# Performance work log

Measured on AMD Instinct MI355X. Metric: run time of the kernel, lower is better.

## Reference

```python
import jax, jax.numpy as jnp
import numpy as np

B, SEQ_LEN, ENC_IN, C_OUT = 128, 512, 21, 21
PRED_LEN, D_MODEL, N_HEADS, D_FF = 96, 512, 8, 2048
E_LAYERS = 2
PATCH_LEN, STRIDE = 16, 8
NUM_PATCH = (SEQ_LEN - PATCH_LEN) // STRIDE + 1  # 63
MODES = min(32, NUM_PATCH // 2)  # 31 (mode_select='low' -> index = range(MODES))
K_MA = 25
EPS = 1e-5
DH = D_MODEL // N_HEADS  # 64


def setup_inputs() -> dict:
    key = jax.random.key(0)
    ks = jax.random.split(key, 16)
    s = 0.02
    fscale = 1.0 / (D_MODEL * D_MODEL)
    return {
        'x_enc': jax.random.normal(ks[0], (B, SEQ_LEN, ENC_IN), jnp.float32),
        'x_mark_enc': jax.random.normal(ks[1], (B, SEQ_LEN, 4), jnp.float32),
        'x_dec': jax.random.normal(ks[2], (B, 144, ENC_IN), jnp.float32),
        'x_mark_dec': jax.random.normal(ks[3], (B, 144, 4), jnp.float32),
        'patch_W': s * jax.random.normal(ks[4], (D_MODEL, PATCH_LEN * ENC_IN), jnp.float32),
        'patch_b': jnp.zeros((D_MODEL,), jnp.float32),
        'Wq': s * jax.random.normal(ks[5], (E_LAYERS, D_MODEL, D_MODEL), jnp.float32),
        'bq': jnp.zeros((E_LAYERS, D_MODEL), jnp.float32),
        'Wo': s * jax.random.normal(ks[6], (E_LAYERS, D_MODEL, D_MODEL), jnp.float32),
        'bo': jnp.zeros((E_LAYERS, D_MODEL), jnp.float32),
        'four_wr': fscale * jax.random.uniform(ks[7], (E_LAYERS, N_HEADS, DH, DH, MODES), jnp.float32),
        'four_wi': fscale * jax.random.uniform(ks[8], (E_LAYERS, N_HEADS, DH, DH, MODES), jnp.float32),
        'conv1_W': s * jax.random.normal(ks[9], (E_LAYERS, D_FF, D_MODEL), jnp.float32),
        'conv2_W': s * jax.random.normal(ks[10], (E_LAYERS, D_MODEL, D_FF), jnp.float32),
        'norm_gamma': jnp.ones((D_MODEL,), jnp.float32),
        'norm_beta': jnp.zeros((D_MODEL,), jnp.float32),
        'head_W': s * jax.random.normal(ks[11], (PRED_LEN * C_OUT, NUM_PATCH * D_MODEL), jnp.float32),
        'head_b': jnp.zeros((PRED_LEN * C_OUT,), jnp.float32),
        'trend_W': s * jax.random.normal(ks[12], (PRED_LEN, SEQ_LEN), jnp.float32),
        'trend_b': jnp.zeros((PRED_LEN,), jnp.float32),
    }


def series_decomp(x, k=K_MA):
    # x: [B, L, C]; replicate-pad ends by (k-1)//2, moving mean via cumsum
    pad = (k - 1) // 2
    front = jnp.repeat(x[:, :1, :], pad, axis=1)
    end = jnp.repeat(x[:, -1:, :], pad, axis=1)
    xp = jnp.concatenate([front, x, end], axis=1)
    c = jnp.cumsum(xp, axis=1)
    c = jnp.concatenate([jnp.zeros_like(c[:, :1]), c], axis=1)
    mean = (c[:, k:] - c[:, :-k]) / k
    return x - mean, mean


def my_layernorm(x, g, b):
    mu = x.mean(-1, keepdims=True)
    var = ((x - mu) ** 2).mean(-1, keepdims=True)
    xh = (x - mu) / jnp.sqrt(var + EPS) * g + b
    return xh - xh.mean(axis=1, keepdims=True)


def fourier_block(q, wr, wi):
    # q: [B, L, H, E] -> torch FourierBlock (low-freq modes 0..MODES-1)
    Bq, L, H, E = q.shape
    xs = q.transpose(0, 2, 3, 1)                       # [B,H,E,L]
    x_ft = jnp.fft.rfft(xs, axis=-1)                   # [B,H,E,L//2+1]
    W = wr + 1j * wi                                   # [H,E,F,M] complex
    out_sel = jnp.einsum('bhem,hefm->bhfm', x_ft[..., :MODES], W)
    out_ft = jnp.zeros(x_ft.shape, x_ft.dtype).at[..., :MODES].set(out_sel)
    y = jnp.fft.irfft(out_ft, n=L, axis=-1)            # [B,H,E,L]
    # torch does out.view(B, L, -1) on contiguous [B,H,E,L]; flat reshape is identical
    return y.reshape(Bq, L, H * E)


def encoder_layer(x, Wq_l, bq_l, Wo_l, bo_l, wr, wi, c1, c2):
    Bq, L, D = x.shape
    q = (x @ Wq_l.T + bq_l).reshape(Bq, L, N_HEADS, DH)
    new_x = fourier_block(q, wr, wi) @ Wo_l.T + bo_l
    x, _ = series_decomp(x + new_x)
    y = jax.nn.gelu(x @ c1.T, approximate=False) @ c2.T  # conv1d k=1 == matmul, no bias
    res, _ = series_decomp(x + y)
    return res


def _forward(x_enc, patch_W, patch_b, Wq, bq, Wo, bo, four_wr, four_wi,
             conv1_W, conv2_W, norm_gamma, norm_beta, head_W, head_b, trend_W, trend_b):
    seasonal, trend = series_decomp(x_enc)
    # trend_projection over time axis: [B,L,C] -> [B,P,C]
    trend_out = jnp.einsum('blc,pl->bpc', trend, trend_W) + trend_b[None, :, None]
    # patching (unfold over time per channel, then mix channels)
    xs = seasonal.transpose(0, 2, 1)                   # [B,N,L]
    idx = STRIDE * jnp.arange(NUM_PATCH)[:, None] + jnp.arange(PATCH_LEN)[None, :]
    xp = xs[:, :, idx]                                 # [B,N,P,plen]
    xp = xp.transpose(0, 2, 1, 3).reshape(B, NUM_PATCH, ENC_IN * PATCH_LEN)
    enc = xp @ patch_W.T + patch_b                     # [B,P,D]
    for l in range(E_LAYERS):
        enc = encoder_layer(enc, Wq[l], bq[l], Wo[l], bo[l],
                            four_wr[l], four_wi[l], conv1_W[l], conv2_W[l])
    enc = my_layernorm(enc, norm_gamma, norm_beta)
    seasonal_out = (enc.reshape(B, -1) @ head_W.T + head_b).reshape(B, PRED_LEN, C_OUT)
    return seasonal_out + trend_out


def reference(x_enc, x_mark_enc, x_dec, x_mark_dec, patch_W, patch_b, Wq, bq, Wo, bo,
              four_wr, four_wi, conv1_W, conv2_W, norm_gamma, norm_beta,
              head_W, head_b, trend_W, trend_b):
    # x_mark_enc / x_dec / x_mark_dec are accepted but unused, as in the torch forward
    return _forward(x_enc, patch_W, patch_b, Wq, bq, Wo, bo, four_wr, four_wi,
                    conv1_W, conv2_W, norm_gamma, norm_beta, head_W, head_b, trend_W, trend_b)
```

## Files before the change

### kernel.cpp

```cpp
#include <hip/hip_runtime.h>
#include <math.h>

#define B_ 128
#define T_ 512
#define C_ 21
#define L_ 63
#define D_ 512
#define H_ 8
#define DH_ 64
#define MODES_ 31
#define FF_ 2048
#define P_ 96
#define KMA 25
#define PAD 12
#define NOUT (P_*C_)
#define KHEAD (L_*D_)
#define ML (B_*L_)

typedef __attribute__((ext_vector_type(8))) short short8;
typedef __attribute__((ext_vector_type(4))) float f32x4;

__device__ __forceinline__ unsigned short f2b(float f) {
    union { float f; unsigned u; } v; v.f = f;
    unsigned r = v.u + 0x7FFFu + ((v.u >> 16) & 1u);
    return (unsigned short)(r >> 16);
}
__device__ __forceinline__ float b2f(unsigned short u) {
    union { unsigned u; float f; } v; v.u = ((unsigned)u) << 16;
    return v.f;
}
__device__ __forceinline__ void gld_lds16(const void* g, void* l) {
    __builtin_amdgcn_global_load_lds(
        (const __attribute__((address_space(1))) unsigned int*)g,
        (__attribute__((address_space(3))) unsigned int*)l, 16, 0, 0);
}

__global__ void prep_k(const float* __restrict__ Wq, const float* __restrict__ Wo,
                       const float* __restrict__ c1, const float* __restrict__ c2,
                       unsigned short* __restrict__ WqB, unsigned short* __restrict__ WoB,
                       unsigned short* __restrict__ c1B, unsigned short* __restrict__ c2B,
                       const float* __restrict__ pW, unsigned short* __restrict__ pWB,
                       float* __restrict__ cosT, float* __restrict__ sinT) {
    int i = blockIdx.x * 256 + threadIdx.x;
    if (i < 262144) {
        const float* src = (i < 131072) ? Wq : Wo;
        unsigned short* dst = (i < 131072) ? WqB : WoB;
        int j = i & 131071;
        float4 v = ((const float4*)src)[j];
        uint2 p; p.x = (unsigned)f2b(v.x) | ((unsigned)f2b(v.y) << 16);
        p.y = (unsigned)f2b(v.z) | ((unsigned)f2b(v.w) << 16);
        ((uint2*)dst)[j] = p;
    } else if (i < 1310720) {
        int j = i - 262144;
        const float* src = (j < 524288) ? c1 : c2;
        unsigned short* dst = (j < 524288) ? c1B : c2B;
        j &= 524287;
        float4 v = ((const float4*)src)[j];
        uint2 p; p.x = (unsigned)f2b(v.x) | ((unsigned)f2b(v.y) << 16);
        p.y = (unsigned)f2b(v.z) | ((unsigned)f2b(v.w) << 16);
        ((uint2*)dst)[j] = p;
    } else if (i < 1359872) {
        int j = i - 1310720;
        int row = j / 96, c4 = j % 96;
        uint2 p; p.x = 0; p.y = 0;
        if (c4 < 84) {
            float4 v = *(const float4*)(pW + (size_t)row * 336 + c4 * 4);
            p.x = (unsigned)f2b(v.x) | ((unsigned)f2b(v.y) << 16);
            p.y = (unsigned)f2b(v.z) | ((unsigned)f2b(v.w) << 16);
        }
        ((uint2*)pWB)[j] = p;
    } else if (i < 1361888) {
        int j = i - 1359872;
        int m = j / 63, l = j % 63;
        if (m >= MODES_) { cosT[j] = 0.f; sinT[j] = 0.f; }
        else {
            int r = (m * l) % 63;
            double a = 6.283185307179586476925286766559 * (double)r / 63.0;
            cosT[j] = (float)cos(a); sinT[j] = (float)sin(a);
        }
    }
}

__global__ void decomp_input_k(const float* __restrict__ x,
                               unsigned short* __restrict__ seasB,
                               unsigned short* __restrict__ trendB) {
    int idx = blockIdx.x * 256 + threadIdx.x;
    if (idx >= B_ * C_ * 16) return;
    int tc = idx & 15; int rc = idx >> 4; int c = rc % C_; int b = rc / C_;
    const float* xb = x + (size_t)b * T_ * C_ + c;
    int t0 = tc * 32;
    float sum = 0.f;
    #pragma unroll
    for (int i = -PAD; i <= PAD; ++i) {
        int tt = t0 + i; tt = tt < 0 ? 0 : (tt > T_-1 ? T_-1 : tt);
        sum += xb[(size_t)tt * C_];
    }
    for (int t = t0; t < t0 + 32; ++t) {
        float mean = sum * (1.f / KMA);
        float xv = xb[(size_t)t * C_];
        size_t o = ((size_t)b * T_ + t) * C_ + c;
        seasB[o]  = f2b(xv - mean);
        trendB[o] = f2b(mean);
        int add = t + 13 > T_-1 ? T_-1 : t + 13;
        int rem = t - 12 < 0 ? 0 : t - 12;
        sum += xb[(size_t)add * C_] - xb[(size_t)rem * C_];
    }
}

__global__ void patches_k(const unsigned short* __restrict__ seasB,
                          unsigned short* __restrict__ xpB) {
    int idx = blockIdx.x * 256 + threadIdx.x;
    if (idx >= B_*L_*384) return;
    int col = idx % 384; int r = idx / 384; int n = r % L_; int b = r / L_;
    unsigned short v = 0;
    if (col < 336) {
        int c = col >> 4; int j = col & 15;
        v = seasB[((size_t)b * T_ + 8*n + j) * C_ + c];
    }
    xpB[idx] = v;
}

__global__ __launch_bounds__(256) void trend_mfma(
    const unsigned short* __restrict__ trendB, const float* __restrict__ tW,
    const float* __restrict__ tb, const float* __restrict__ hb,
    float* __restrict__ outT)
{
    __shared__ unsigned short Asl[64*32];
    __shared__ unsigned short Wsl[96*32];
    int bm = blockIdx.x;
    int t = threadIdx.x, wave = t >> 6, lane = t & 63;
    int wr = wave >> 1, wc = wave & 1, g2 = lane >> 4, rl = lane & 15;
    f32x4 acc[2][3] = {};
    int ar = t >> 2, aslot = t & 3;
    int rowg = bm*64 + ar; int ab = rowg / 21, ac = rowg % 21;
    for (int k0 = 0; k0 < 512; k0 += 32) {
        __syncthreads();
        {
            unsigned short vals[8];
            int kb = k0 + aslot*8;
            #pragma unroll
            for (int j = 0; j < 8; ++j)
                vals[j] = trendB[((size_t)ab * T_ + kb + j) * C_ + ac];
            int phys = aslot ^ ((ar>>1)&3);
            *(uint4*)&Asl[ar*32 + phys*8] = *(const uint4*)vals;
        }
        #pragma unroll
        for (int i = 0; i < 3; ++i) {
            int idx = t + 256*i;
            int r = idx >> 3, c4 = idx & 7;
            float4 w4 = *(const float4*)(tW + (size_t)r * T_ + k0 + c4*4);
            uint2 p; p.x = (unsigned)f2b(w4.x) | ((unsigned)f2b(w4.y) << 16);
            p.y = (unsigned)f2b(w4.z) | ((unsigned)f2b(w4.w) << 16);
            *(uint2*)&Wsl[r*32 + (((c4>>1) ^ ((r>>1)&3)) << 3) + ((c4&1) << 2)] = p;
        }
        __syncthreads();
        short8 af[2], wf[3];
        #pragma unroll
        for (int m = 0; m < 2; ++m) {
            int r = wr*32 + m*16 + rl;
            af[m] = *(const short8*)&Asl[r*32 + ((g2 ^ ((r>>1)&3)) << 3)];
        }
        #pragma unroll
        for (int n = 0; n < 3; ++n) {
            int r = wc*48 + n*16 + rl;
            wf[n] = *(const short8*)&Wsl[r*32 + ((g2 ^ ((r>>1)&3)) << 3)];
        }
        #pragma unroll
        for (int m = 0; m < 2; ++m)
            #pragma unroll
            for (int n = 0; n < 3; ++n)
                acc[m][n] = __builtin_amdgcn_mfma_f32_16x16x32_bf16(af[m], wf[n], acc[m][n], 0,0,0);
    }
    #pragma unroll
    for (int n = 0; n < 3; ++n) {
        int p = wc*48 + n*16 + rl;
        float bias = tb[p];
        #pragma unroll
        for (int m = 0; m < 2; ++m)
            #pragma unroll
            for (int j = 0; j < 4; ++j) {
                int rg = bm*64 + wr*32 + m*16 + g2*4 + j;
                int b = rg / 21, c = rg % 21;
                outT[(size_t)b * NOUT + p*21 + c] = acc[m][n][j] + bias + hb[p*21 + c];
            }
    }
}

__global__ __launch_bounds__(256) void gemm_mfma(
    const unsigned short* __restrict__ A,
    const unsigned short* __restrict__ W,
    const float* __restrict__ bias,
    float* __restrict__ Cf,
    unsigned short* __restrict__ Cb,
    int M, int N, int K, int act)
{
    __shared__ unsigned short Asl[64*64];
    __shared__ unsigned short Wsl[128*64];
    int bm = blockIdx.y, bn = blockIdx.x;
    int t = threadIdx.x;
    int wave = t >> 6, lane = t & 63;
    int wr = wave >> 1, wc = wave & 1;
    int g2 = lane >> 4, rl = lane & 15;
    int lr8 = lane >> 3, l7 = lane & 7;
    f32x4 acc[2][4] = {};
    const unsigned short* Ab = A + (size_t)(bm*64) * K;
    const unsigned short* Wb = W + (size_t)(bn*128) * K;

    for (int k0 = 0; k0 < K; k0 += 64) {
        __syncthreads();
        #pragma unroll
        for (int i = 0; i < 2; ++i) {
            int seg = wave*2 + i;
            int r = seg*8 + lr8;
            int ko = (l7 ^ (r & 7)) << 3;
            gld_lds16(Ab + (size_t)r*K + k0 + ko, &Asl[seg*512]);
        }
        #pragma unroll
        for (int i = 0; i < 4; ++i) {
            int seg = wave*4 + i;
            int r = seg*8 + lr8;
            int ko = (l7 ^ (r & 7)) << 3;
            gld_lds16(Wb + (size_t)r*K + k0 + ko, &Wsl[seg*512]);
        }
        __syncthreads();
        short8 af[2][2], wf[2][4];
        #pragma unroll
        for (int sub = 0; sub < 2; ++sub) {
            #pragma unroll
            for (int m = 0; m < 2; ++m) {
                int r = wr*32 + m*16 + rl;
                af[sub][m] = *(const short8*)&Asl[r*64 + (((sub*4+g2) ^ (r&7)) << 3)];
            }
            #pragma unroll
            for (int n = 0; n < 4; ++n) {
                int r = wc*64 + n*16 + rl;
                wf[sub][n] = *(const short8*)&Wsl[r*64 + (((sub*4+g2) ^ (r&7)) << 3)];
            }
        }
        #pragma unroll
        for (int sub = 0; sub < 2; ++sub)
            #pragma unroll
            for (int m = 0; m < 2; ++m)
                #pragma unroll
                for (int n = 0; n < 4; ++n)
                    acc[m][n] = __builtin_amdgcn_mfma_f32_16x16x32_bf16(af[sub][m], wf[sub][n], acc[m][n], 0,0,0);
    }

    int crow0 = bm*64 + wr*32;
    int ccol0 = bn*128 + wc*64;
    #pragma unroll
    for (int n = 0; n < 4; ++n) {
        int col = ccol0 + n*16 + rl;
        float bv = bias ? bias[col] : 0.f;
        #pragma unroll
        for (int m = 0; m < 2; ++m) {
            #pragma unroll
            for (int j = 0; j < 4; ++j) {
                int row = crow0 + m*16 + g2*4 + j;
                float x = acc[m][n][j] + bv;
                if (act == 1) x = 0.5f * x * (1.f + erff(x * 0.70710678118654752f));
                size_t ix = (size_t)row * N + col;
                if (Cf) Cf[ix] = x;
                if (Cb) Cb[ix] = f2b(x);
            }
        }
    }
}

__global__ __launch_bounds__(256) void fourier1_k(
    const float* __restrict__ q, const float* __restrict__ cosT, const float* __restrict__ sinT,
    float* __restrict__ Xre_g, float* __restrict__ Xim_g)
{
    __shared__ float qs[63][64];
    __shared__ float ct[2016], st[2016];
    int b = blockIdx.x >> 3, h = blockIdx.x & 7;
    int t = threadIdx.x;
    for (int idx = t; idx < 1008; idx += 256) {
        int l = idx >> 4, e4 = idx & 15;
        *(float4*)&qs[l][e4*4] = *(const float4*)(q + ((size_t)(b*63 + l))*512 + h*64 + e4*4);
    }
    for (int idx = t; idx < 504; idx += 256) {
        *(float4*)&ct[idx*4] = *(const float4*)(cosT + idx*4);
        *(float4*)&st[idx*4] = *(const float4*)(sinT + idx*4);
    }
    __syncthreads();
    int mm = t & 31, g = t >> 5;
    float re[8] = {}, im[8] = {};
    for (int l = 0; l < 63; ++l) {
        float c = ct[mm*63 + l], s = st[mm*63 + l];
        #pragma unroll
        for (int j = 0; j < 8; ++j) {
            float v = qs[l][g*8 + j];
            re[j] = fmaf(v, c, re[j]);
            im[j] = fmaf(-v, s, im[j]);
        }
    }
    if (mm < MODES_) {
        size_t base = ((size_t)(h*MODES_ + mm)*128 + b)*64 + g*8;
        *(float4*)&Xre_g[base]   = *(float4*)&re[0];
        *(float4*)&Xre_g[base+4] = *(float4*)&re[4];
        *(float4*)&Xim_g[base]   = *(float4*)&im[0];
        *(float4*)&Xim_g[base+4] = *(float4*)&im[4];
    }
}

__global__ __launch_bounds__(256) void fourier2_k(
    const float* __restrict__ Xre_g, const float* __restrict__ Xim_g,
    const float* __restrict__ wr, const float* __restrict__ wi,
    float* __restrict__ Ore_g, float* __restrict__ Oim_g)
{
    __shared__ unsigned short Xr[128*64], Xi[128*64];
    __shared__ unsigned short Wr[64*64], Wi[64*64], Wn[64*64];
    int h = blockIdx.x / MODES_, mm = blockIdx.x % MODES_;
    int t = threadIdx.x;
    size_t xbase = ((size_t)(h*MODES_ + mm)) * 128 * 64;
    #pragma unroll
    for (int i = 0; i < 8; ++i) {
        int idx = t + 256*i;
        int r = idx >> 4, c4 = idx & 15;
        int ad = r*64 + (((c4>>1) ^ (r&7)) << 3) + ((c4&1) << 2);
        float4 v = *(const float4*)(Xre_g + xbase + (size_t)r*64 + c4*4);
        uint2 p; p.x = (unsigned)f2b(v.x) | ((unsigned)f2b(v.y) << 16);
        p.y = (unsigned)f2b(v.z) | ((unsigned)f2b(v.w) << 16);
        *(uint2*)&Xr[ad] = p;
        v = *(const float4*)(Xim_g + xbase + (size_t)r*64 + c4*4);
        p.x = (unsigned)f2b(v.x) | ((unsigned)f2b(v.y) << 16);
        p.y = (unsigned)f2b(v.z) | ((unsigned)f2b(v.w) << 16);
        *(uint2*)&Xi[ad] = p;
    }
    #pragma unroll
    for (int i = 0; i < 2; ++i) {
        int idx = t + 256*i;
        int f = idx >> 3, oct = idx & 7;
        unsigned short wrv[8], wiv[8], wnv[8];
        #pragma unroll
        for (int j = 0; j < 8; ++j) {
            int e = oct*8 + j;
            size_t a = (((size_t)(h*64 + e))*64 + f)*MODES_ + mm;
            wrv[j] = f2b(wr[a]);
            wiv[j] = f2b(wi[a]);
            wnv[j] = wiv[j] ^ 0x8000u;
        }
        int ad = f*64 + ((oct ^ (f&7)) << 3);
        *(uint4*)&Wr[ad] = *(const uint4*)wrv;
        *(uint4*)&Wi[ad] = *(const uint4*)wiv;
        *(uint4*)&Wn[ad] = *(const uint4*)wnv;
    }
    __syncthreads();
    int wave = t >> 6, lane = t & 63;
    int wv = wave >> 1, wc = wave & 1;
    int g2 = lane >> 4, rl = lane & 15;
    f32x4 ar[4][2] = {}, ai[4][2] = {};
    #pragma unroll
    for (int sub = 0; sub < 2; ++sub) {
        short8 xr[4], xi[4], br[2], bi[2], bn[2];
        #pragma unroll
        for (int m = 0; m < 4; ++m) {
            int r = wv*64 + m*16 + rl;
            int off = r*64 + (((sub*4+g2) ^ (r&7)) << 3);
            xr[m] = *(const short8*)&Xr[off];
            xi[m] = *(const short8*)&Xi[off];
        }
        #pragma unroll
        for (int n = 0; n < 2; ++n) {
            int r = wc*32 + n*16 + rl;
            int off = r*64 + (((sub*4+g2) ^ (r&7)) << 3);
            br[n] = *(const short8*)&Wr[off];
            bi[n] = *(const short8*)&Wi[off];
            bn[n] = *(const short8*)&Wn[off];
        }
        #pragma unroll
        for (int m = 0; m < 4; ++m)
            #pragma unroll
            for (int n = 0; n < 2; ++n) {
                ar[m][n] = __builtin_amdgcn_mfma_f32_16x16x32_bf16(xr[m], br[n], ar[m][n], 0,0,0);
                ar[m][n] = __builtin_amdgcn_mfma_f32_16x16x32_bf16(xi[m], bn[n], ar[m][n], 0,0,0);
                ai[m][n] = __builtin_amdgcn_mfma_f32_16x16x32_bf16(xr[m], bi[n], ai[m][n], 0,0,0);
                ai[m][n] = __builtin_amdgcn_mfma_f32_16x16x32_bf16(xi[m], br[n], ai[m][n], 0,0,0);
            }
    }
    #pragma unroll
    for (int m = 0; m < 4; ++m)
        #pragma unroll
        for (int n = 0; n < 2; ++n)
            #pragma unroll
            for (int j = 0; j < 4; ++j) {
                int b = wv*64 + m*16 + g2*4 + j;
                int f = wc*32 + n*16 + rl;
                Ore_g[xbase + (size_t)b*64 + f] = ar[m][n][j];
                Oim_g[xbase + (size_t)b*64 + f] = ai[m][n][j];
            }
}

__global__ __launch_bounds__(256) void fourier3_k(
    const float* __restrict__ Ore_g, const float* __restrict__ Oim_g,
    const float* __restrict__ cosT, const float* __restrict__ sinT,
    unsigned short* __restrict__ yB)
{
    __shared__ float Ore[31][64], Oim[31][64];
    __shared__ float ct[2016], st[2016];
    int b = blockIdx.x >> 3, h = blockIdx.x & 7;
    int t = threadIdx.x;
    for (int idx = t; idx < 496; idx += 256) {
        int m = idx >> 4, e4 = idx & 15;
        size_t a = ((size_t)(h*MODES_ + m)*128 + b)*64 + e4*4;
        *(float4*)&Ore[m][e4*4] = *(const float4*)(Ore_g + a);
        *(float4*)&Oim[m][e4*4] = *(const float4*)(Oim_g + a);
    }
    for (int idx = t; idx < 504; idx += 256) {
        *(float4*)&ct[idx*4] = *(const float4*)(cosT + idx*4);
        *(float4*)&st[idx*4] = *(const float4*)(sinT + idx*4);
    }
    __syncthreads();
    int f = t & 63, w = t >> 6;
    int l0 = w*16;
    float y[16];
    float r0 = Ore[0][f];
    #pragma unroll
    for (int i = 0; i < 16; ++i) y[i] = r0;
    for (int m = 1; m < MODES_; ++m) {
        float re2 = 2.f*Ore[m][f], im2 = 2.f*Oim[m][f];
        #pragma unroll
        for (int i = 0; i < 16; ++i) {
            y[i] = fmaf(re2, ct[m*63 + l0 + i], y[i]);
            y[i] = fmaf(-im2, st[m*63 + l0 + i], y[i]);
        }
    }
    int nl = (w == 3) ? 15 : 16;
    unsigned short* yo = yB + ((size_t)(b*512) + h*64 + f) * 63 + l0;
    for (int i = 0; i < nl; ++i) yo[i] = f2b(y[i] * (1.f/63.f));
}

__global__ void decomp_add_k(const unsigned short* __restrict__ X,
                             const unsigned short* __restrict__ Yv,
                             unsigned short* __restrict__ outB) {
    int idx = blockIdx.x * 256 + threadIdx.x;
    if (idx >= B_*D_) return;
    int b = idx >> 9, d = idx & 511;
    const unsigned short* xp = X  + (size_t)b * L_ * D_ + d;
    const unsigned short* yp = Yv + (size_t)b * L_ * D_ + d;
    unsigned short* ob = outB + (size_t)b * L_ * D_ + d;
    #define RD(l) (b2f(xp[(size_t)(l) * D_]) + b2f(yp[(size_t)(l) * D_]))
    float sum = 13.f * RD(0);
    #pragma unroll
    for (int j = 1; j <= 12; ++j) sum += RD(j);
    for (int l = 0; l < L_; ++l) {
        float res = RD(l) - sum * (1.f / KMA);
        ob[(size_t)l * D_] = f2b(res);
        int add = l + 13 > L_-1 ? L_-1 : l + 13;
        int rem = l - 12 < 0 ? 0 : l - 12;
        sum += RD(add) - RD(rem);
    }
    #undef RD
}

__global__ __launch_bounds__(256) void ln_colmean_k(
    const unsigned short* __restrict__ Xb, const float* __restrict__ g,
    const float* __restrict__ bt, unsigned short* __restrict__ outB)
{
    __shared__ unsigned short lds[63][512];
    int b = blockIdx.x;
    int w = threadIdx.x >> 6, lane = threadIdx.x & 63;
    for (int i = 0; i < 16; ++i) {
        int row = w*16 + i;
        if (row >= 63) break;
        const unsigned short* x = Xb + ((size_t)(b*63 + row))*512 + lane*8;
        uint4 raw = *(const uint4*)x;
        const unsigned short* rp = (const unsigned short*)&raw;
        float v[8]; float s = 0.f, s2 = 0.f;
        #pragma unroll
        for (int j = 0; j < 8; ++j) { v[j] = b2f(rp[j]); s += v[j]; s2 += v[j]*v[j]; }
        #pragma unroll
        for (int o = 32; o > 0; o >>= 1) { s += __shfl_down(s, o); s2 += __shfl_down(s2, o); }
        s = __shfl(s, 0); s2 = __shfl(s2, 0);
        float mu = s * (1.f/D_);
        float var = s2 * (1.f/D_) - mu*mu;
        float rs = rsqrtf(var + 1e-5f);
        unsigned short o16[8];
        #pragma unroll
        for (int j = 0; j < 8; ++j) {
            int d = lane*8 + j;
            o16[j] = f2b((v[j] - mu) * rs * g[d] + bt[d]);
        }
        *(uint4*)&lds[row][lane*8] = *(const uint4*)o16;
    }
    __syncthreads();
    #pragma unroll
    for (int i = 0; i < 2; ++i) {
        int d = threadIdx.x + 256*i;
        float s = 0.f;
        for (int l = 0; l < 63; ++l) s += b2f(lds[l][d]);
        s *= (1.f / 63.f);
        for (int l = 0; l < 63; ++l)
            outB[((size_t)(b*63 + l))*512 + d] = f2b(b2f(lds[l][d]) - s);
    }
}

__global__ __launch_bounds__(256) void head_mfma(
    const unsigned short* __restrict__ A,
    const float* __restrict__ W,
    float* __restrict__ parts)
{
    __shared__ unsigned short Asl[128*32];
    __shared__ unsigned short Wsl[48*32];
    int nt = blockIdx.x;
    int kc = blockIdx.y;
    int t = threadIdx.x;
    int wave = t >> 6, lane = t & 63;
    int g2 = lane >> 4, rl = lane & 15;
    int srow = lane >> 2, sslot = lane & 3;
    f32x4 acc[2][3] = {};
    int k0base = kc * 2688;
    float4 w4c[2];
    {
        #pragma unroll
        for (int i = 0; i < 2; ++i) {
            int idx = t + 256*i;
            if (idx < 384) {
                int r = idx >> 3, c4 = idx & 7;
                w4c[i] = *(const float4*)(W + (size_t)(nt*48 + r)*KHEAD + k0base + c4*4);
            }
        }
    }
    for (int ks = 0; ks < 84; ++ks) {
        int k0 = k0base + ks*32;
        __syncthreads();
        #pragma unroll
        for (int i = 0; i < 2; ++i) {
            int idx = t + 256*i;
            if (idx < 384) {
                int r = idx >> 3, c4 = idx & 7;
                uint2 p; p.x = (unsigned)f2b(w4c[i].x) | ((unsigned)f2b(w4c[i].y) << 16);
                p.y = (unsigned)f2b(w4c[i].z) | ((unsigned)f2b(w4c[i].w) << 16);
                *(uint2*)&Wsl[r*32 + (((c4>>1) ^ ((r>>1)&3)) << 3) + ((c4&1) << 2)] = p;
            }
        }
        #pragma unroll
        for (int i = 0; i < 2; ++i) {
            int seg = wave*2 + i;
            int rA = seg*16 + srow;
            int koA = (sslot ^ ((rA>>1)&3)) << 3;
            gld_lds16(A + (size_t)rA * KHEAD + k0 + koA, &Asl[seg*512]);
        }
        __syncthreads();
        float4 w4n[2];
        if (ks < 83) {
            int k1 = k0 + 32;
            #pragma unroll
            for (int i = 0; i < 2; ++i) {
                int idx = t + 256*i;
                if (idx < 384) {
                    int r = idx >> 3, c4 = idx & 7;
                    w4n[i] = *(const float4*)(W + (size_t)(nt*48 + r)*KHEAD + k1 + c4*4);
                }
            }
        }
        short8 af[2], wf[3];
        #pragma unroll
        for (int m = 0; m < 2; ++m) {
            int r = wave*32 + m*16 + rl;
            af[m] = *(const short8*)&Asl[r*32 + ((g2 ^ ((r>>1)&3)) << 3)];
        }
        #pragma unroll
        for (int n = 0; n < 3; ++n) {
            int r = n*16 + rl;
            wf[n] = *(const short8*)&Wsl[r*32 + ((g2 ^ ((r>>1)&3)) << 3)];
        }
        #pragma unroll
        for (int m = 0; m < 2; ++m)
            #pragma unroll
            for (int n = 0; n < 3; ++n)
                acc[m][n] = __builtin_amdgcn_mfma_f32_16x16x32_bf16(af[m], wf[n], acc[m][n], 0,0,0);
        if (ks < 83) { w4c[0] = w4n[0]; w4c[1] = w4n[1]; }
    }
    float* pout = parts + (size_t)kc * B_ * NOUT;
    #pragma unroll
    for (int n = 0; n < 3; ++n) {
        int col = nt*48 + n*16 + rl;
        #pragma unroll
        for (int m = 0; m < 2; ++m)
            #pragma unroll
            for (int j = 0; j < 4; ++j) {
                int row = wave*32 + m*16 + g2*4 + j;
                pout[(size_t)row * NOUT + col] = acc[m][n][j];
            }
    }
}

__global__ void reduce_k(const float* __restrict__ trendout, const float* __restrict__ parts,
                         float* __restrict__ out) {
    int i = blockIdx.x * 256 + threadIdx.x;
    if (i >= 64512) return;
    float4 s = ((const float4*)trendout)[i];
    for (int kc = 0; kc < 12; ++kc) {
        float4 p = ((const float4*)parts)[(size_t)kc * 64512 + i];
        s.x += p.x; s.y += p.y; s.z += p.z; s.w += p.w;
    }
    ((float4*)out)[i] = s;
}

extern "C" void kernel_launch(void* const* d_in, const int* in_sizes, int n_in,
                              void* d_out, int out_size, void* d_ws, size_t ws_size,
                              hipStream_t stream) {
    const float* x_enc   = (const float*)d_in[0];
    const float* patch_W = (const float*)d_in[4];
    const float* patch_b = (const float*)d_in[5];
    const float* Wq      = (const float*)d_in[6];
    const float* bq      = (const float*)d_in[7];
    const float* Wo      = (const float*)d_in[8];
    const float* bo      = (const float*)d_in[9];
    const float* four_wr = (const float*)d_in[10];
    const float* four_wi = (const float*)d_in[11];
    const float* c1      = (const float*)d_in[12];
    const float* c2      = (const float*)d_in[13];
    const float* gamma   = (const float*)d_in[14];
    const float* beta    = (const float*)d_in[15];
    const float* head_W  = (const float*)d_in[16];
    const float* head_b  = (const float*)d_in[17];
    const float* trend_W = (const float*)d_in[18];
    const float* trend_b = (const float*)d_in[19];
    float* out = (float*)d_out;
    float* ws  = (float*)d_ws;

    unsigned short* seasB  = (unsigned short*)ws;
    unsigned short* trendB = (unsigned short*)(ws + 688128);
    unsigned short* xpB    = (unsigned short*)(ws + 1376256);
    unsigned short* bufAb  = (unsigned short*)(ws + 2924544);
    unsigned short* tmpB16 = (unsigned short*)(ws + 4988928);
    unsigned short* tmp2   = (unsigned short*)(ws + 7053312);
    unsigned short* bufCb  = (unsigned short*)(ws + 9117696);
    float* qF    = ws + 11182080;
    float* Ore_g = qF;
    float* Oim_g = qF + 2031616;
    float* big   = ws + 15310848;
    unsigned short* hidB = (unsigned short*)big;
    float* Xre_g = big;
    float* Xim_g = big + 2031616;
    unsigned short* WqB = (unsigned short*)(ws + 23568384);
    unsigned short* WoB = (unsigned short*)(ws + 23830528);
    unsigned short* c1B = (unsigned short*)(ws + 24092672);
    unsigned short* c2B = (unsigned short*)(ws + 25141248);
    unsigned short* pWB = (unsigned short*)(ws + 26189824);
    float* cosT = ws + 26288128;
    float* sinT = ws + 26290144;
    float* trendout = ws + 26292160;
    float* parts = ws + 26550208;

    auto cdiv = [](int a, int b) { return (a + b - 1) / b; };

    prep_k<<<5321,256,0,stream>>>(Wq, Wo, c1, c2, WqB, WoB, c1B, c2B, patch_W, pWB, cosT, sinT);
    decomp_input_k<<<cdiv(B_*C_*16,256),256,0,stream>>>(x_enc, seasB, trendB);
    patches_k<<<cdiv(B_*L_*384,256),256,0,stream>>>(seasB, xpB);
    trend_mfma<<<42,256,0,stream>>>(trendB, trend_W, trend_b, head_b, trendout);

    gemm_mfma<<<dim3(4,126),256,0,stream>>>(xpB, pWB, patch_b, (float*)nullptr, bufAb, ML, 512, 384, 0);

    for (int l = 0; l < 2; ++l) {
        const unsigned short* WqB_l = WqB + (size_t)l*512*512;
        const unsigned short* WoB_l = WoB + (size_t)l*512*512;
        const unsigned short* c1B_l = c1B + (size_t)l*FF_*D_;
        const unsigned short* c2B_l = c2B + (size_t)l*D_*FF_;
        const float* bq_l = bq + (size_t)l*512;
        const float* bo_l = bo + (size_t)l*512;
        const float* wr_l = four_wr + (size_t)l*H_*DH_*DH_*MODES_;
        const float* wi_l = four_wi + (size_t)l*H_*DH_*DH_*MODES_;

        gemm_mfma<<<dim3(4,126),256,0,stream>>>(bufAb, WqB_l, bq_l, qF, (unsigned short*)nullptr, ML, 512, 512, 0);
        fourier1_k<<<B_*H_,256,0,stream>>>(qF, cosT, sinT, Xre_g, Xim_g);
        fourier2_k<<<H_*MODES_,256,0,stream>>>(Xre_g, Xim_g, wr_l, wi_l, Ore_g, Oim_g);
        fourier3_k<<<B_*H_,256,0,stream>>>(Ore_g, Oim_g, cosT, sinT, tmpB16);
        gemm_mfma<<<dim3(4,126),256,0,stream>>>(tmpB16, WoB_l, bo_l, (float*)nullptr, tmp2, ML, 512, 512, 0);
        decomp_add_k<<<cdiv(B_*D_,256),256,0,stream>>>(bufAb, tmp2, bufCb);
        gemm_mfma<<<dim3(16,126),256,0,stream>>>(bufCb, c1B_l, (const float*)nullptr, (float*)nullptr, hidB, ML, FF_, 512, 1);
        gemm_mfma<<<dim3(4,126),256,0,stream>>>(hidB, c2B_l, (const float*)nullptr, (float*)nullptr, tmp2, ML, 512, FF_, 0);
        decomp_add_k<<<cdiv(B_*D_,256),256,0,stream>>>(bufCb, tmp2, bufAb);
    }

    ln_colmean_k<<<B_,256,0,stream>>>(bufAb, gamma, beta, tmpB16);
    head_mfma<<<dim3(42,12),256,0,stream>>>(tmpB16, head_W, parts);
    reduce_k<<<cdiv(64512,256),256,0,stream>>>(trendout, parts, out);
}
```

Before: 627.4 us.

## Double-buffer GEMM LDS tiles and split head GEMM K across waves

The generic MFMA GEMM now double-buffers its A and W LDS tiles. The next K-tile's global-to-LDS loads are issued before computing on the current tile, and one barrier per iteration is removed. The head GEMM kernel drops LDS staging entirely. Each wave reads A and W fragments straight from global memory over its own quarter of the K chunk, converting W from fp32 to bf16 in registers, and the four waves' partial accumulators are then reduced through a shared buffer. This trades LDS traffic and barriers for uncoalesced direct global loads, larger per-wave accumulator register use (8x3 tiles), and a serialized shared-memory reduction.

Result: faster. 556.1 us, median of 5 (-11.4%).

```diff
diff --git a/kernel.cpp b/kernel.cpp
--- a/kernel.cpp
+++ b/kernel.cpp
@@ -194,8 +194,8 @@
     unsigned short* __restrict__ Cb,
     int M, int N, int K, int act)
 {
-    __shared__ unsigned short Asl[64*64];
-    __shared__ unsigned short Wsl[128*64];
+    __shared__ unsigned short Asl[2][64*64];
+    __shared__ unsigned short Wsl[2][128*64];
     int bm = blockIdx.y, bn = blockIdx.x;
     int t = threadIdx.x;
     int wave = t >> 6, lane = t & 63;
@@ -206,35 +206,53 @@
     const unsigned short* Ab = A + (size_t)(bm*64) * K;
     const unsigned short* Wb = W + (size_t)(bn*128) * K;
 
-    for (int k0 = 0; k0 < K; k0 += 64) {
+    #pragma unroll
+    for (int i = 0; i < 2; ++i) {
+        int seg = wave*2 + i;
+        int r = seg*8 + lr8;
+        int ko = (l7 ^ (r & 7)) << 3;
+        gld_lds16(Ab + (size_t)r*K + ko, &Asl[0][seg*512]);
+    }
+    #pragma unroll
+    for (int i = 0; i < 4; ++i) {
+        int seg = wave*4 + i;
+        int r = seg*8 + lr8;
+        int ko = (l7 ^ (r & 7)) << 3;
+        gld_lds16(Wb + (size_t)r*K + ko, &Wsl[0][seg*512]);
+    }
+
+    int cur = 0;
+    for (int k0 = 0; k0 < K; k0 += 64, cur ^= 1) {
         __syncthreads();
-        #pragma unroll
-        for (int i = 0; i < 2; ++i) {
-            int seg = wave*2 + i;
-            int r = seg*8 + lr8;
-            int ko = (l7 ^ (r & 7)) << 3;
-            gld_lds16(Ab + (size_t)r*K + k0 + ko, &Asl[seg*512]);
-        }
-        #pragma unroll
-        for (int i = 0; i < 4; ++i) {
-            int seg = wave*4 + i;
-            int r = seg*8 + lr8;
-            int ko = (l7 ^ (r & 7)) << 3;
-            gld_lds16(Wb + (size_t)r*K + k0 + ko, &Wsl[seg*512]);
-        }
-        __syncthreads();
+        if (k0 + 64 < K) {
+            int kn = k0 + 64;
+            #pragma unroll
+            for (int i = 0; i < 2; ++i) {
+                int seg = wave*2 + i;
+                int r = seg*8 + lr8;
+                int ko = (l7 ^ (r & 7)) << 3;
+                gld_lds16(Ab + (size_t)r*K + kn + ko, &Asl[cur^1][seg*512]);
+            }
+            #pragma unroll
+            for (int i = 0; i < 4; ++i) {
+                int seg = wave*4 + i;
+                int r = seg*8 + lr8;
+                int ko = (l7 ^ (r & 7)) << 3;
+                gld_lds16(Wb + (size_t)r*K + kn + ko, &Wsl[cur^1][seg*512]);
+            }
+        }
         short8 af[2][2], wf[2][4];
         #pragma unroll
         for (int sub = 0; sub < 2; ++sub) {
             #pragma unroll
             for (int m = 0; m < 2; ++m) {
                 int r = wr*32 + m*16 + rl;
-                af[sub][m] = *(const short8*)&Asl[r*64 + (((sub*4+g2) ^ (r&7)) << 3)];
+                af[sub][m] = *(const short8*)&Asl[cur][r*64 + (((sub*4+g2) ^ (r&7)) << 3)];
             }
             #pragma unroll
             for (int n = 0; n < 4; ++n) {
                 int r = wc*64 + n*16 + rl;
-                wf[sub][n] = *(const short8*)&Wsl[r*64 + (((sub*4+g2) ^ (r&7)) << 3)];
+                wf[sub][n] = *(const short8*)&Wsl[cur][r*64 + (((sub*4+g2) ^ (r&7)) << 3)];
             }
         }
         #pragma unroll
@@ -501,89 +519,57 @@
     const float* __restrict__ W,
     float* __restrict__ parts)
 {
-    __shared__ unsigned short Asl[128*32];
-    __shared__ unsigned short Wsl[48*32];
+    __shared__ float red[128][48];
     int nt = blockIdx.x;
     int kc = blockIdx.y;
-    int t = threadIdx.x;
-    int wave = t >> 6, lane = t & 63;
-    int g2 = lane >> 4, rl = lane & 15;
-    int srow = lane >> 2, sslot = lane & 3;
-    f32x4 acc[2][3] = {};
-    int k0base = kc * 2688;
-    float4 w4c[2];
-    {
-        #pragma unroll
-        for (int i = 0; i < 2; ++i) {
-            int idx = t + 256*i;
-            if (idx < 384) {
-                int r = idx >> 3, c4 = idx & 7;
-                w4c[i] = *(const float4*)(W + (size_t)(nt*48 + r)*KHEAD + k0base + c4*4);
-            }
-        }
-    }
-    for (int ks = 0; ks < 84; ++ks) {
-        int k0 = k0base + ks*32;
-        __syncthreads();
-        #pragma unroll
-        for (int i = 0; i < 2; ++i) {
-            int idx = t + 256*i;
-            if (idx < 384) {
-                int r = idx >> 3, c4 = idx & 7;
-                uint2 p; p.x = (unsigned)f2b(w4c[i].x) | ((unsigned)f2b(w4c[i].y) << 16);
-                p.y = (unsigned)f2b(w4c[i].z) | ((unsigned)f2b(w4c[i].w) << 16);
-                *(uint2*)&Wsl[r*32 + (((c4>>1) ^ ((r>>1)&3)) << 3) + ((c4&1) << 2)] = p;
-            }
-        }
-        #pragma unroll
-        for (int i = 0; i < 2; ++i) {
-            int seg = wave*2 + i;
-            int rA = seg*16 + srow;
-            int koA = (sslot ^ ((rA>>1)&3)) << 3;
-            gld_lds16(A + (size_t)rA * KHEAD + k0 + koA, &Asl[seg*512]);
-        }
-        __syncthreads();
-        float4 w4n[2];
-        if (ks < 83) {
-            int k1 = k0 + 32;
-            #pragma unroll
-            for (int i = 0; i < 2; ++i) {
-                int idx = t + 256*i;
-                if (idx < 384) {
-                    int r = idx >> 3, c4 = idx & 7;
-                    w4n[i] = *(const float4*)(W + (size_t)(nt*48 + r)*KHEAD + k1 + c4*4);
-                }
-            }
-        }
-        short8 af[2], wf[3];
-        #pragma unroll
-        for (int m = 0; m < 2; ++m) {
-            int r = wave*32 + m*16 + rl;
-            af[m] = *(const short8*)&Asl[r*32 + ((g2 ^ ((r>>1)&3)) << 3)];
-        }
+    int wv = threadIdx.x >> 6, lane = threadIdx.x & 63;
+    int rl = lane & 15, g2 = lane >> 4;
+    f32x4 acc[8][3] = {};
+    const unsigned short* Ab = A + (size_t)rl * KHEAD;
+    const float* Wb = W + (size_t)(nt*48 + rl) * KHEAD;
+    int kbeg = kc*2688 + wv*672 + g2*8;
+
+    for (int ks = 0; ks < 21; ++ks) {
+        int k = kbeg + ks*32;
+        short8 af[8];
+        #pragma unroll
+        for (int m = 0; m < 8; ++m)
+            af[m] = *(const short8*)(Ab + (size_t)(m*16) * KHEAD + k);
+        short8 wf[3];
         #pragma unroll
         for (int n = 0; n < 3; ++n) {
-            int r = n*16 + rl;
-            wf[n] = *(const short8*)&Wsl[r*32 + ((g2 ^ ((r>>1)&3)) << 3)];
-        }
-        #pragma unroll
-        for (int m = 0; m < 2; ++m)
+            float4 lo = *(const float4*)(Wb + (size_t)(n*16) * KHEAD + k);
+            float4 hi = *(const float4*)(Wb + (size_t)(n*16) * KHEAD + k + 4);
+            unsigned short u[8] = { f2b(lo.x), f2b(lo.y), f2b(lo.z), f2b(lo.w),
+                                    f2b(hi.x), f2b(hi.y), f2b(hi.z), f2b(hi.w) };
+            wf[n] = *(const short8*)u;
+        }
+        #pragma unroll
+        for (int m = 0; m < 8; ++m)
             #pragma unroll
             for (int n = 0; n < 3; ++n)
                 acc[m][n] = __builtin_amdgcn_mfma_f32_16x16x32_bf16(af[m], wf[n], acc[m][n], 0,0,0);
-        if (ks < 83) { w4c[0] = w4n[0]; w4c[1] = w4n[1]; }
-    }
-    float* pout = parts + (size_t)kc * B_ * NOUT;
-    #pragma unroll
-    for (int n = 0; n < 3; ++n) {
-        int col = nt*48 + n*16 + rl;
-        #pragma unroll
-        for (int m = 0; m < 2; ++m)
-            #pragma unroll
-            for (int j = 0; j < 4; ++j) {
-                int row = wave*32 + m*16 + g2*4 + j;
-                pout[(size_t)row * NOUT + col] = acc[m][n][j];
-            }
+    }
+
+    for (int w = 0; w < 4; ++w) {
+        if (wv == w) {
+            #pragma unroll
+            for (int m = 0; m < 8; ++m)
+                #pragma unroll
+                for (int n = 0; n < 3; ++n)
+                    #pragma unroll
+                    for (int j = 0; j < 4; ++j) {
+                        int row = m*16 + g2*4 + j, col = n*16 + rl;
+                        if (w == 0) red[row][col] = acc[m][n][j];
+                        else        red[row][col] += acc[m][n][j];
+                    }
+        }
+        __syncthreads();
+    }
+    float* pout = parts + (size_t)kc * (B_*NOUT);
+    for (int idx = threadIdx.x; idx < 128*48; idx += 256) {
+        int row = idx / 48, col = idx % 48;
+        pout[(size_t)row * NOUT + nt*48 + col] = red[row][col];
     }
 }
 
```
